# Performance work log

Hardware: AMD Instinct MI355X
Metric: run time of the kernel (lower is better)

## Reference

```python
import jax, jax.numpy as jnp
import numpy as np

# Static config (matches init_kwargs / spatial layout)
SHAPES = ((64, 64), (32, 32), (16, 16))   # (H, W) per level, bev=256 at /4,/8,/16
B, HEADS, LEVELS, POINTS, C = 2, 8, 3, 4, 256
HD = C // HEADS
NV = sum(h * w for h, w in SHAPES)        # 5376
NQ = NV
TP = HEADS * LEVELS * POINTS              # 96


def setup_inputs() -> dict:
    key = jax.random.key(0)
    ks = jax.random.split(key, 10)
    s = 1.0 / np.sqrt(C)
    inp = {
        'query': jax.random.normal(ks[0], (B, NQ, C), dtype=jnp.float32),
        'reference_points': jax.random.uniform(ks[1], (B, NQ, 2), dtype=jnp.float32),
        'value': jax.random.normal(ks[2], (B, NV, C), dtype=jnp.float32),
        'Wv': jax.random.normal(ks[3], (C, C), dtype=jnp.float32) * s,
        'bv': jnp.zeros((C,), dtype=jnp.float32),
        # offset proj: small scale so sampling stays local-ish (orig init is 0)
        'Woff': jax.random.normal(ks[4], (TP * 2, C), dtype=jnp.float32) * (0.02 * s),
        'boff': jnp.zeros((TP * 2,), dtype=jnp.float32),
        'Wa': jax.random.normal(ks[5], (TP, C), dtype=jnp.float32) * s,
        'ba': jnp.zeros((TP,), dtype=jnp.float32),
        'Wo': jax.random.normal(ks[6], (C, C), dtype=jnp.float32) * s,
        'bo': jnp.zeros((C,), dtype=jnp.float32),
    }
    return inp


def _msda(query, reference_points, value, Wv, bv, Woff, boff, Wa, ba, Wo, bo):
    Bb, nq, _ = query.shape
    # value projection -> per-head values
    v = (value @ Wv.T + bv).reshape(Bb, NV, HEADS, HD)
    # sampling offsets: (B, NQ, HEADS, LEVELS, POINTS, 2)
    off = (query @ Woff.T + boff).reshape(Bb, nq, HEADS, LEVELS, POINTS, 2)
    # attention weights: softmax over LEVELS*POINTS jointly
    a = (query @ Wa.T + ba).reshape(Bb, nq, HEADS, LEVELS * POINTS)
    a = jax.nn.softmax(a, axis=-1).reshape(Bb, nq, HEADS, LEVELS, POINTS)
    # sampling locations in [0,1] (clamp matches torch .clamp(0,1))
    loc = jnp.clip(reference_points[:, :, None, None, None, :] + off, 0.0, 1.0)

    out = jnp.zeros((Bb, HEADS, nq, HD), dtype=query.dtype)
    start = 0
    for lvl, (H, W) in enumerate(SHAPES):
        n = H * W
        # (B, HEADS, H*W, HD) flattened level feature map per head
        vl = jnp.transpose(v[:, start:start + n].reshape(Bb, H, W, HEADS, HD),
                           (0, 3, 1, 2, 4)).reshape(Bb, HEADS, n, HD)
        loc_l = loc[:, :, :, lvl]                     # (B, NQ, HEADS, K, 2)
        # align_corners=False unnormalization: ((g+1)*size - 1)/2 with g=2*loc-1
        x = loc_l[..., 0] * W - 0.5
        y = loc_l[..., 1] * H - 0.5
        x0 = jnp.floor(x)
        y0 = jnp.floor(y)
        wx1 = x - x0
        wy1 = y - y0
        x0i = x0.astype(jnp.int32)
        y0i = y0.astype(jnp.int32)
        acc = jnp.zeros((Bb, HEADS, nq * POINTS, HD), dtype=query.dtype)
        for dy in (0, 1):
            for dx in (0, 1):
                ix = x0i + dx
                iy = y0i + dy
                wgt = (wx1 if dx else 1.0 - wx1) * (wy1 if dy else 1.0 - wy1)
                # zero padding outside the map (padding_mode='zeros')
                valid = (ix >= 0) & (ix < W) & (iy >= 0) & (iy < H)
                idx = jnp.clip(iy, 0, H - 1) * W + jnp.clip(ix, 0, W - 1)
                idx_t = jnp.transpose(idx, (0, 2, 1, 3)).reshape(Bb, HEADS, nq * POINTS)
                g = jnp.take_along_axis(vl, idx_t[..., None], axis=2)  # (B,H,NQ*K,HD)
                w_t = jnp.transpose(wgt * valid.astype(wgt.dtype),
                                    (0, 2, 1, 3)).reshape(Bb, HEADS, nq * POINTS, 1)
                acc = acc + g * w_t
        aw = jnp.transpose(a[:, :, :, lvl], (0, 2, 1, 3)).reshape(Bb, HEADS, nq * POINTS, 1)
        out = out + (acc * aw).reshape(Bb, HEADS, nq, POINTS, HD).sum(axis=3)
        start += n
    out = jnp.transpose(out, (0, 2, 1, 3)).reshape(Bb, nq, C)
    return out @ Wo.T + bo


def reference(query, reference_points, value, Wv, bv, Woff, boff, Wa, ba, Wo, bo):
    return _msda(query, reference_points, value, Wv, bv, Woff, boff, Wa, ba, Wo, bo)
```

## Files before the change

### kernel.cpp

```cpp
#include <hip/hip_runtime.h>
#include <hip/hip_bf16.h>
#include <cmath>

#define BATCH   2
#define NQ      5376
#define NV      5376
#define CDIM    256
#define HEADS   8
#define HD      32
#define LEVELS  3
#define POINTS  4
#define TP      96
#define MROWS   (BATCH*NQ)
#define NOFF    (TP*2)
#define NQA     (NOFF+TP)
#define N4_VQ   (MROWS*CDIM/4)

typedef __attribute__((ext_vector_type(8))) short bf16x8;
typedef __attribute__((ext_vector_type(4))) float f32x4;
typedef unsigned short u16;
typedef unsigned int   u32;

#define AS1 __attribute__((address_space(1)))
#define AS3 __attribute__((address_space(3)))

__device__ __forceinline__ void g2lds16(const void* g, void* l) {
    __builtin_amdgcn_global_load_lds((const AS1 void*)g, (AS3 void*)l, 16, 0, 0);
}

__device__ __forceinline__ u16 bf_of(float f) {
    union { __hip_bfloat16 h; u16 s; } u;
    u.h = __float2bfloat16(f);
    return u.s;
}
__device__ __forceinline__ float bf_back(u16 s) {
    return __uint_as_float((u32)s << 16);
}

__global__ __launch_bounds__(256) void split_all_kernel(
    const float* __restrict__ value, const float* __restrict__ query,
    const float* __restrict__ Wv, const float* __restrict__ Woff,
    const float* __restrict__ Wa, const float* __restrict__ Wo,
    u16* __restrict__ vhi, u16* __restrict__ vlo, u16* __restrict__ qhi,
    u16* __restrict__ wv_hi, u16* __restrict__ wv_lo,
    u16* __restrict__ wqa_hi,
    u16* __restrict__ wo_hi, u16* __restrict__ wo_lo)
{
    const int i = blockIdx.x * 256 + threadIdx.x;
    int j; const float* src; u16 *dh, *dl;
    if (i < N4_VQ) {
        j = i; src = value + (size_t)j * 4; dh = vhi; dl = vlo;
    } else if (i < 2 * N4_VQ) {
        j = i - N4_VQ; src = query + (size_t)j * 4; dh = qhi; dl = nullptr;
    } else if (i < 2 * N4_VQ + 16384) {
        j = i - 2 * N4_VQ; src = Wv + (size_t)j * 4; dh = wv_hi; dl = wv_lo;
    } else if (i < 2 * N4_VQ + 34816) {
        j = i - 2 * N4_VQ - 16384;
        const int row = j >> 6, c4 = j & 63;
        src = (row < NOFF) ? (Woff + (size_t)row * CDIM + c4 * 4)
                           : (Wa + (size_t)(row - NOFF) * CDIM + c4 * 4);
        dh = wqa_hi; dl = nullptr;
    } else {
        j = i - 2 * N4_VQ - 34816; src = Wo + (size_t)j * 4; dh = wo_hi; dl = wo_lo;
    }
    const float4 v = *reinterpret_cast<const float4*>(src);
    ushort4 h;
    h.x = bf_of(v.x); h.y = bf_of(v.y); h.z = bf_of(v.z); h.w = bf_of(v.w);
    reinterpret_cast<ushort4*>(dh)[j] = h;
    if (dl) {
        ushort4 l;
        l.x = bf_of(v.x - bf_back(h.x));
        l.y = bf_of(v.y - bf_back(h.y));
        l.z = bf_of(v.z - bf_back(h.z));
        l.w = bf_of(v.w - bf_back(h.w));
        reinterpret_cast<ushort4*>(dl)[j] = l;
    }
}

#define GBM 64
#define GBN 64
#define GBK 32

template <int NPROD, int MODE>
__device__ __forceinline__ void gemm_body(
    int m0, int n0,
    const u16* __restrict__ Ah, const u16* __restrict__ Al,
    const u16* __restrict__ Bh, const u16* __restrict__ Bl,
    const float* __restrict__ bias, const float* __restrict__ bias2,
    void* __restrict__ Cout, void* __restrict__ Cout2,
    int N, int K,
    u16* sAh, u16* sAl, u16* sBh, u16* sBl)
{
    const int tid  = threadIdx.x;
    const int lane = tid & 63;
    const int wave = tid >> 6;
    const int wr   = wave & 1;
    const int wc   = wave >> 1;
    const int qm   = lane & 15;
    const int quad = lane >> 4;

    f32x4 acc[2][2];
    #pragma unroll
    for (int i = 0; i < 2; ++i)
        #pragma unroll
        for (int j = 0; j < 2; ++j)
            acc[i][j] = (f32x4){0.f, 0.f, 0.f, 0.f};

    const int srow = (wave << 4) + (lane >> 2);
    const int sk   = (lane & 3) * 8;
    const int brc  = min(n0 + srow, N - 1);

    for (int k0 = 0; k0 < K; k0 += GBK) {
        const size_t ga = (size_t)(m0 + srow) * K + k0 + sk;
        const size_t gb = (size_t)brc * K + k0 + sk;
        g2lds16(Ah + ga, sAh + wave * 512);
        if (NPROD >= 2) g2lds16(Al + ga, sAl + wave * 512);
        g2lds16(Bh + gb, sBh + wave * 512);
        __syncthreads();

        bf16x8 fah[2], fal[2], fbh[2];
        #pragma unroll
        for (int x = 0; x < 2; ++x) {
            const int rm = wr * 32 + x * 16 + qm;
            const int rn = wc * 32 + x * 16 + qm;
            fah[x] = *reinterpret_cast<const bf16x8*>(&sAh[rm * GBK + quad * 8]);
            fbh[x] = *reinterpret_cast<const bf16x8*>(&sBh[rn * GBK + quad * 8]);
            if (NPROD >= 2)
                fal[x] = *reinterpret_cast<const bf16x8*>(&sAl[rm * GBK + quad * 8]);
        }
        #pragma unroll
        for (int mi = 0; mi < 2; ++mi)
            #pragma unroll
            for (int ni = 0; ni < 2; ++ni) {
                acc[mi][ni] = __builtin_amdgcn_mfma_f32_16x16x32_bf16(
                    fah[mi], fbh[ni], acc[mi][ni], 0, 0, 0);
                if (NPROD >= 2)
                    acc[mi][ni] = __builtin_amdgcn_mfma_f32_16x16x32_bf16(
                        fal[mi], fbh[ni], acc[mi][ni], 0, 0, 0);
            }
        __syncthreads();
    }

    #pragma unroll
    for (int mi = 0; mi < 2; ++mi) {
        #pragma unroll
        for (int ni = 0; ni < 2; ++ni) {
            const int n = n0 + wc * 32 + ni * 16 + qm;
            if (n >= N) continue;
            float bn;
            if (MODE == 2) bn = (n < NOFF) ? bias[n] : bias2[n - NOFF];
            else           bn = bias[n];
            #pragma unroll
            for (int r = 0; r < 4; ++r) {
                const int m = m0 + wr * 32 + mi * 16 + quad * 4 + r;
                const float val = acc[mi][ni][r] + bn;
                if (MODE == 0) {
                    reinterpret_cast<float*>(Cout)[(size_t)m * N + n] = val;
                } else if (MODE == 1) {
                    const int b = m / NV, rr = m - b * NV;
                    const int h = n >> 5, c = n & 31;
                    reinterpret_cast<u16*>(Cout)[
                        (((size_t)b * HEADS + h) * NV + rr) * HD + c] = bf_of(val);
                } else {
                    if (n < NOFF)
                        reinterpret_cast<float*>(Cout)[(size_t)m * NOFF + n] = val;
                    else
                        reinterpret_cast<float*>(Cout2)[(size_t)m * TP + (n - NOFF)] = val;
                }
            }
        }
    }
}

#define VBLOCKS (168 * 4)
__global__ __launch_bounds__(256) void gemm_vqa_kernel(
    const u16* __restrict__ vAh, const u16* __restrict__ vAl,
    const u16* __restrict__ vBh, const float* __restrict__ vbias,
    u16* __restrict__ vOut,
    const u16* __restrict__ qAh, const u16* __restrict__ qBh,
    const float* __restrict__ qb1, const float* __restrict__ qb2,
    float* __restrict__ qOut1, float* __restrict__ qOut2)
{
    __shared__ u16 sAh[GBM * GBK];
    __shared__ u16 sAl[GBM * GBK];
    __shared__ u16 sBh[GBN * GBK];
    const int bid = blockIdx.x;
    if (bid < VBLOCKS) {
        const int nt = bid & 3, mt = bid >> 2;
        gemm_body<2, 1>(mt * GBM, nt * GBN, vAh, vAl, vBh, nullptr,
                        vbias, nullptr, vOut, nullptr, CDIM, CDIM,
                        sAh, sAl, sBh, nullptr);
    } else {
        const int b2 = bid - VBLOCKS;
        const int nt = b2 % 5, mt = b2 / 5;
        gemm_body<1, 2>(mt * GBM, nt * GBN, qAh, nullptr, qBh, nullptr,
                        qb1, qb2, qOut1, qOut2, NQA, CDIM,
                        sAh, sAl, sBh, nullptr);
    }
}

__global__ __launch_bounds__(256) void gemm_out_kernel(
    const u16* __restrict__ Ah, const u16* __restrict__ Al,
    const u16* __restrict__ Bh, const float* __restrict__ bias,
    float* __restrict__ Cout)
{
    __shared__ u16 sAh[GBM * GBK];
    __shared__ u16 sAl[GBM * GBK];
    __shared__ u16 sBh[GBN * GBK];
    const int bid = blockIdx.x;
    const int nt = bid & 3, mt = bid >> 2;
    gemm_body<2, 0>(mt * GBM, nt * GBN, Ah, Al, Bh, nullptr,
                    bias, nullptr, Cout, nullptr, CDIM, CDIM,
                    sAh, sAl, sBh, nullptr);
}

__global__ __launch_bounds__(256) void msda_core_kernel(
    const float* __restrict__ off,
    const float* __restrict__ alog,
    const float* __restrict__ refp,
    const u16*   __restrict__ v,
    u16* __restrict__ t_hi,
    u16* __restrict__ t_lo)
{
    const int tid  = threadIdx.x;
    const int half = tid >> 7;
    const int ht   = tid & 127;
    const int bq   = blockIdx.x * 2 + half;
    const int b    = bq / NQ;

    __shared__ float s_w[2][TP];
    __shared__ int   s_idx[2][TP][4];
    __shared__ float s_twt[2][TP][4];

    if (ht < TP) s_w[half][ht] = alog[(size_t)bq * TP + ht];
    __syncthreads();

    if (ht < HEADS) {
        float mx = -1e30f;
        #pragma unroll
        for (int i = 0; i < 12; ++i) mx = fmaxf(mx, s_w[half][ht * 12 + i]);
        float e[12];
        float sum = 0.f;
        #pragma unroll
        for (int i = 0; i < 12; ++i) {
            e[i] = expf(s_w[half][ht * 12 + i] - mx);
            sum += e[i];
        }
        const float inv = 1.f / sum;
        #pragma unroll
        for (int i = 0; i < 12; ++i) s_w[half][ht * 12 + i] = e[i] * inv;
    }
    __syncthreads();

    if (ht < TP) {
        const int j  = ht;
        const int jj = j % 12;
        const int l  = jj >> 2;
        const int Wl    = (l == 0) ? 64 : (l == 1) ? 32 : 16;
        const int start = (l == 0) ? 0 : (l == 1) ? 4096 : 5120;

        const float refx = refp[(size_t)bq * 2 + 0];
        const float refy = refp[(size_t)bq * 2 + 1];
        const float lx = fminf(fmaxf(refx + off[(size_t)bq * NOFF + j * 2 + 0], 0.f), 1.f) * (float)Wl - 0.5f;
        const float ly = fminf(fmaxf(refy + off[(size_t)bq * NOFF + j * 2 + 1], 0.f), 1.f) * (float)Wl - 0.5f;
        const float fx0 = floorf(lx), fy0 = floorf(ly);
        const int   x0  = (int)fx0,   y0  = (int)fy0;
        const float wx1 = lx - fx0,   wy1 = ly - fy0;
        const float wx0 = 1.f - wx1,  wy0 = 1.f - wy1;
        const float aw  = s_w[half][j];

        #pragma unroll
        for (int k = 0; k < 4; ++k) {
            const int dx = k & 1, dy = k >> 1;
            const int xi = x0 + dx, yi = y0 + dy;
            const bool ok = (xi >= 0) & (xi < Wl) & (yi >= 0) & (yi < Wl);
            const int xc = min(max(xi, 0), Wl - 1);
            const int yc = min(max(yi, 0), Wl - 1);
            s_idx[half][j][k] = (start + yc * Wl + xc) * (HD * 2);
            const float wxy = (dx ? wx1 : wx0) * (dy ? wy1 : wy0);
            s_twt[half][j][k] = ok ? aw * wxy : 0.f;
        }
    }
    __syncthreads();

    const int h   = ht >> 4;
    const int sub = ht & 15;
    const int q   = sub & 7;
    const int rep = sub >> 3;
    const char* vb = (const char*)v + (((size_t)b * HEADS + h) * NV) * (HD * 2) + q * 8;

    float acc0 = 0.f, acc1 = 0.f, acc2 = 0.f, acc3 = 0.f;
    #pragma unroll
    for (int g = 0; g < 3; ++g) {
        uint2 raw[8];
        float wt[8];
        #pragma unroll
        for (int pp = 0; pp < 2; ++pp) {
            const int j = h * 12 + rep * 6 + g * 2 + pp;
            const int4   ix = *reinterpret_cast<const int4*>(&s_idx[half][j][0]);
            const float4 tw = *reinterpret_cast<const float4*>(&s_twt[half][j][0]);
            raw[pp * 4 + 0] = *reinterpret_cast<const uint2*>(vb + ix.x);
            raw[pp * 4 + 1] = *reinterpret_cast<const uint2*>(vb + ix.y);
            raw[pp * 4 + 2] = *reinterpret_cast<const uint2*>(vb + ix.z);
            raw[pp * 4 + 3] = *reinterpret_cast<const uint2*>(vb + ix.w);
            wt[pp * 4 + 0] = tw.x; wt[pp * 4 + 1] = tw.y;
            wt[pp * 4 + 2] = tw.z; wt[pp * 4 + 3] = tw.w;
        }
        #pragma unroll
        for (int k = 0; k < 8; ++k) {
            acc0 += wt[k] * __uint_as_float(raw[k].x << 16);
            acc1 += wt[k] * __uint_as_float(raw[k].x & 0xffff0000u);
            acc2 += wt[k] * __uint_as_float(raw[k].y << 16);
            acc3 += wt[k] * __uint_as_float(raw[k].y & 0xffff0000u);
        }
    }

    acc0 += __shfl_xor(acc0, 8);
    acc1 += __shfl_xor(acc1, 8);
    acc2 += __shfl_xor(acc2, 8);
    acc3 += __shfl_xor(acc3, 8);

    if (rep == 0) {
        ushort4 hh, ll;
        hh.x = bf_of(acc0); ll.x = bf_of(acc0 - bf_back(hh.x));
        hh.y = bf_of(acc1); ll.y = bf_of(acc1 - bf_back(hh.y));
        hh.z = bf_of(acc2); ll.z = bf_of(acc2 - bf_back(hh.z));
        hh.w = bf_of(acc3); ll.w = bf_of(acc3 - bf_back(hh.w));
        const size_t base = (size_t)bq * CDIM + h * HD + q * 4;
        *reinterpret_cast<ushort4*>(t_hi + base) = hh;
        *reinterpret_cast<ushort4*>(t_lo + base) = ll;
    }
}

extern "C" void kernel_launch(void* const* d_in, const int* in_sizes, int n_in,
                              void* d_out, int out_size, void* d_ws, size_t ws_size,
                              hipStream_t stream)
{
    const float* query = (const float*)d_in[0];
    const float* refp  = (const float*)d_in[1];
    const float* value = (const float*)d_in[2];
    const float* Wv    = (const float*)d_in[3];
    const float* bv    = (const float*)d_in[4];
    const float* Woff  = (const float*)d_in[5];
    const float* boff  = (const float*)d_in[6];
    const float* Wa    = (const float*)d_in[7];
    const float* ba    = (const float*)d_in[8];
    const float* Wo    = (const float*)d_in[9];
    const float* bo    = (const float*)d_in[10];
    float* out = (float*)d_out;

    char* w = (char*)d_ws;
    const size_t SZ_QV = (size_t)MROWS * CDIM * 2;
    u16* q_hi   = (u16*)(w);
    u16* val_hi = (u16*)(w + 1 * SZ_QV);
    u16* val_lo = (u16*)(w + 2 * SZ_QV);
    u16* v_bf16 = (u16*)(w + 3 * SZ_QV);
    char* wp    = w + 4 * SZ_QV;
    u16* wv_hi  = (u16*)(wp);                  wp += (size_t)CDIM * CDIM * 2;
    u16* wv_lo  = (u16*)(wp);                  wp += (size_t)CDIM * CDIM * 2;
    u16* wqa_hi = (u16*)(wp);                  wp += (size_t)NQA * CDIM * 2;
    u16* wo_hi  = (u16*)(wp);                  wp += (size_t)CDIM * CDIM * 2;
    u16* wo_lo  = (u16*)(wp);                  wp += (size_t)CDIM * CDIM * 2;
    float* ws_off = (float*)(wp);              wp += (size_t)MROWS * NOFF * 4;
    float* ws_a   = (float*)(wp);
    u16* t_hi = val_hi;
    u16* t_lo = val_lo;

    const dim3 blk(256);

    split_all_kernel<<<dim3((2 * N4_VQ + 51200) / 256), blk, 0, stream>>>(
        value, query, Wv, Woff, Wa, Wo,
        val_hi, val_lo, q_hi, wv_hi, wv_lo, wqa_hi, wo_hi, wo_lo);

    gemm_vqa_kernel<<<dim3(VBLOCKS + (MROWS / GBM) * 5), blk, 0, stream>>>(
        val_hi, val_lo, wv_hi, bv, v_bf16,
        q_hi, wqa_hi, boff, ba, ws_off, ws_a);

    msda_core_kernel<<<dim3(MROWS / 2), blk, 0, stream>>>(
        ws_off, ws_a, refp, v_bf16, t_hi, t_lo);

    gemm_out_kernel<<<dim3((MROWS / GBM) * 4), blk, 0, stream>>>(
        t_hi, t_lo, wo_hi, bo, out);
}
```

Baseline: 140.6 us.

## Fuse fp32-to-bf16 split conversion into GEMM tile loads, store offsets/logits as bf16

Removes the separate split_all kernel. The value/query GEMM and the output GEMM now read fp32 inputs and weights directly and convert them to bf16 hi/lo while staging tiles into LDS. This drops one launch and the round trip of writing and re-reading the bf16 copies. The offset and attention-logit outputs are also stored as bf16 instead of fp32, halving that intermediate traffic at the cost of lower precision in the sampling locations and softmax inputs. In exchange, the async global_load_lds path is replaced by register loads plus conversion for the fused operands, and weights are re-converted in every block.

```diff
diff --git a/kernel.cpp b/kernel.cpp
--- a/kernel.cpp
+++ b/kernel.cpp
@@ -14,7 +14,6 @@
 #define MROWS   (BATCH*NQ)
 #define NOFF    (TP*2)
 #define NQA     (NOFF+TP)
-#define N4_VQ   (MROWS*CDIM/4)
 
 typedef __attribute__((ext_vector_type(8))) short bf16x8;
 typedef __attribute__((ext_vector_type(4))) float f32x4;
@@ -37,60 +36,45 @@
     return __uint_as_float((u32)s << 16);
 }
 
-__global__ __launch_bounds__(256) void split_all_kernel(
-    const float* __restrict__ value, const float* __restrict__ query,
-    const float* __restrict__ Wv, const float* __restrict__ Woff,
-    const float* __restrict__ Wa, const float* __restrict__ Wo,
-    u16* __restrict__ vhi, u16* __restrict__ vlo, u16* __restrict__ qhi,
-    u16* __restrict__ wv_hi, u16* __restrict__ wv_lo,
-    u16* __restrict__ wqa_hi,
-    u16* __restrict__ wo_hi, u16* __restrict__ wo_lo)
-{
-    const int i = blockIdx.x * 256 + threadIdx.x;
-    int j; const float* src; u16 *dh, *dl;
-    if (i < N4_VQ) {
-        j = i; src = value + (size_t)j * 4; dh = vhi; dl = vlo;
-    } else if (i < 2 * N4_VQ) {
-        j = i - N4_VQ; src = query + (size_t)j * 4; dh = qhi; dl = nullptr;
-    } else if (i < 2 * N4_VQ + 16384) {
-        j = i - 2 * N4_VQ; src = Wv + (size_t)j * 4; dh = wv_hi; dl = wv_lo;
-    } else if (i < 2 * N4_VQ + 34816) {
-        j = i - 2 * N4_VQ - 16384;
-        const int row = j >> 6, c4 = j & 63;
-        src = (row < NOFF) ? (Woff + (size_t)row * CDIM + c4 * 4)
-                           : (Wa + (size_t)(row - NOFF) * CDIM + c4 * 4);
-        dh = wqa_hi; dl = nullptr;
-    } else {
-        j = i - 2 * N4_VQ - 34816; src = Wo + (size_t)j * 4; dh = wo_hi; dl = wo_lo;
-    }
-    const float4 v = *reinterpret_cast<const float4*>(src);
+__device__ __forceinline__ ushort4 cvt_hi(float4 v) {
     ushort4 h;
     h.x = bf_of(v.x); h.y = bf_of(v.y); h.z = bf_of(v.z); h.w = bf_of(v.w);
-    reinterpret_cast<ushort4*>(dh)[j] = h;
-    if (dl) {
-        ushort4 l;
-        l.x = bf_of(v.x - bf_back(h.x));
-        l.y = bf_of(v.y - bf_back(h.y));
-        l.z = bf_of(v.z - bf_back(h.z));
-        l.w = bf_of(v.w - bf_back(h.w));
-        reinterpret_cast<ushort4*>(dl)[j] = l;
-    }
+    return h;
+}
+__device__ __forceinline__ ushort4 cvt_lo(float4 v, ushort4 h) {
+    ushort4 l;
+    l.x = bf_of(v.x - bf_back(h.x));
+    l.y = bf_of(v.y - bf_back(h.y));
+    l.z = bf_of(v.z - bf_back(h.z));
+    l.w = bf_of(v.w - bf_back(h.w));
+    return l;
 }
 
 #define GBM 64
 #define GBN 64
 #define GBK 32
 
-template <int NPROD, int MODE>
-__device__ __forceinline__ void gemm_body(
-    int m0, int n0,
-    const u16* __restrict__ Ah, const u16* __restrict__ Al,
-    const u16* __restrict__ Bh, const u16* __restrict__ Bl,
-    const float* __restrict__ bias, const float* __restrict__ bias2,
-    void* __restrict__ Cout, void* __restrict__ Cout2,
-    int N, int K,
-    u16* sAh, u16* sAl, u16* sBh, u16* sBl)
+
+#define VBLOCKS (168 * 4)
+__global__ __launch_bounds__(256) void gemm_vqa_kernel(
+    const float* __restrict__ value, const float* __restrict__ Wv,
+    const float* __restrict__ bv, u16* __restrict__ vOut,
+    const float* __restrict__ query, const float* __restrict__ Woff,
+    const float* __restrict__ Wa,
+    const float* __restrict__ boff, const float* __restrict__ ba,
+    u16* __restrict__ offOut, u16* __restrict__ aOut)
 {
+    __shared__ u16 sAh[GBM * GBK];
+    __shared__ u16 sAl[GBM * GBK];
+    __shared__ u16 sBh[GBN * GBK];
+
+    const int bid = blockIdx.x;
+    const bool vpath = bid < VBLOCKS;
+    int m0, n0;
+    if (vpath) { m0 = (bid >> 2) * GBM;           n0 = (bid & 3) * GBN; }
+    else       { const int b2 = bid - VBLOCKS;
+                 m0 = (b2 / 5) * GBM;             n0 = (b2 % 5) * GBN; }
+
     const int tid  = threadIdx.x;
     const int lane = tid & 63;
     const int wave = tid >> 6;
@@ -99,6 +83,19 @@
     const int qm   = lane & 15;
     const int quad = lane >> 4;
 
+    const int srow = tid >> 2;
+    const int sc   = (tid & 3) * 8;
+
+    const float* Asrc = (vpath ? value : query) + (size_t)(m0 + srow) * CDIM;
+    const float* Bsrc;
+    if (vpath) {
+        Bsrc = Wv + (size_t)(n0 + srow) * CDIM;
+    } else {
+        const int rg = min(n0 + srow, NQA - 1);
+        Bsrc = (rg < NOFF) ? (Woff + (size_t)rg * CDIM)
+                           : (Wa + (size_t)(rg - NOFF) * CDIM);
+    }
+
     f32x4 acc[2][2];
     #pragma unroll
     for (int i = 0; i < 2; ++i)
@@ -106,16 +103,20 @@
         for (int j = 0; j < 2; ++j)
             acc[i][j] = (f32x4){0.f, 0.f, 0.f, 0.f};
 
-    const int srow = (wave << 4) + (lane >> 2);
-    const int sk   = (lane & 3) * 8;
-    const int brc  = min(n0 + srow, N - 1);
-
-    for (int k0 = 0; k0 < K; k0 += GBK) {
-        const size_t ga = (size_t)(m0 + srow) * K + k0 + sk;
-        const size_t gb = (size_t)brc * K + k0 + sk;
-        g2lds16(Ah + ga, sAh + wave * 512);
-        if (NPROD >= 2) g2lds16(Al + ga, sAl + wave * 512);
-        g2lds16(Bh + gb, sBh + wave * 512);
+    for (int k0 = 0; k0 < CDIM; k0 += GBK) {
+        const float4 a0 = *reinterpret_cast<const float4*>(&Asrc[k0 + sc]);
+        const float4 a1 = *reinterpret_cast<const float4*>(&Asrc[k0 + sc + 4]);
+        const ushort4 ah0 = cvt_hi(a0), ah1 = cvt_hi(a1);
+        *reinterpret_cast<ushort4*>(&sAh[srow * GBK + sc])     = ah0;
+        *reinterpret_cast<ushort4*>(&sAh[srow * GBK + sc + 4]) = ah1;
+        if (vpath) {
+            *reinterpret_cast<ushort4*>(&sAl[srow * GBK + sc])     = cvt_lo(a0, ah0);
+            *reinterpret_cast<ushort4*>(&sAl[srow * GBK + sc + 4]) = cvt_lo(a1, ah1);
+        }
+        const float4 b0 = *reinterpret_cast<const float4*>(&Bsrc[k0 + sc]);
+        const float4 b1 = *reinterpret_cast<const float4*>(&Bsrc[k0 + sc + 4]);
+        *reinterpret_cast<ushort4*>(&sBh[srow * GBK + sc])     = cvt_hi(b0);
+        *reinterpret_cast<ushort4*>(&sBh[srow * GBK + sc + 4]) = cvt_hi(b1);
         __syncthreads();
 
         bf16x8 fah[2], fal[2], fbh[2];
@@ -125,7 +126,7 @@
             const int rn = wc * 32 + x * 16 + qm;
             fah[x] = *reinterpret_cast<const bf16x8*>(&sAh[rm * GBK + quad * 8]);
             fbh[x] = *reinterpret_cast<const bf16x8*>(&sBh[rn * GBK + quad * 8]);
-            if (NPROD >= 2)
+            if (vpath)
                 fal[x] = *reinterpret_cast<const bf16x8*>(&sAl[rm * GBK + quad * 8]);
         }
         #pragma unroll
@@ -134,7 +135,7 @@
             for (int ni = 0; ni < 2; ++ni) {
                 acc[mi][ni] = __builtin_amdgcn_mfma_f32_16x16x32_bf16(
                     fah[mi], fbh[ni], acc[mi][ni], 0, 0, 0);
-                if (NPROD >= 2)
+                if (vpath)
                     acc[mi][ni] = __builtin_amdgcn_mfma_f32_16x16x32_bf16(
                         fal[mi], fbh[ni], acc[mi][ni], 0, 0, 0);
             }
@@ -146,77 +147,116 @@
         #pragma unroll
         for (int ni = 0; ni < 2; ++ni) {
             const int n = n0 + wc * 32 + ni * 16 + qm;
-            if (n >= N) continue;
-            float bn;
-            if (MODE == 2) bn = (n < NOFF) ? bias[n] : bias2[n - NOFF];
-            else           bn = bias[n];
-            #pragma unroll
-            for (int r = 0; r < 4; ++r) {
-                const int m = m0 + wr * 32 + mi * 16 + quad * 4 + r;
-                const float val = acc[mi][ni][r] + bn;
-                if (MODE == 0) {
-                    reinterpret_cast<float*>(Cout)[(size_t)m * N + n] = val;
-                } else if (MODE == 1) {
+            if (vpath) {
+                const float bn = bv[n];
+                #pragma unroll
+                for (int r = 0; r < 4; ++r) {
+                    const int m = m0 + wr * 32 + mi * 16 + quad * 4 + r;
+                    const float val = acc[mi][ni][r] + bn;
                     const int b = m / NV, rr = m - b * NV;
                     const int h = n >> 5, c = n & 31;
-                    reinterpret_cast<u16*>(Cout)[
-                        (((size_t)b * HEADS + h) * NV + rr) * HD + c] = bf_of(val);
-                } else {
+                    vOut[(((size_t)b * HEADS + h) * NV + rr) * HD + c] = bf_of(val);
+                }
+            } else {
+                if (n >= NQA) continue;
+                const float bn = (n < NOFF) ? boff[n] : ba[n - NOFF];
+                #pragma unroll
+                for (int r = 0; r < 4; ++r) {
+                    const int m = m0 + wr * 32 + mi * 16 + quad * 4 + r;
+                    const float val = acc[mi][ni][r] + bn;
                     if (n < NOFF)
-                        reinterpret_cast<float*>(Cout)[(size_t)m * NOFF + n] = val;
+                        offOut[(size_t)m * NOFF + n] = bf_of(val);
                     else
-                        reinterpret_cast<float*>(Cout2)[(size_t)m * TP + (n - NOFF)] = val;
+                        aOut[(size_t)m * TP + (n - NOFF)] = bf_of(val);
                 }
             }
         }
     }
 }
 
-#define VBLOCKS (168 * 4)
-__global__ __launch_bounds__(256) void gemm_vqa_kernel(
-    const u16* __restrict__ vAh, const u16* __restrict__ vAl,
-    const u16* __restrict__ vBh, const float* __restrict__ vbias,
-    u16* __restrict__ vOut,
-    const u16* __restrict__ qAh, const u16* __restrict__ qBh,
-    const float* __restrict__ qb1, const float* __restrict__ qb2,
-    float* __restrict__ qOut1, float* __restrict__ qOut2)
-{
-    __shared__ u16 sAh[GBM * GBK];
-    __shared__ u16 sAl[GBM * GBK];
-    __shared__ u16 sBh[GBN * GBK];
-    const int bid = blockIdx.x;
-    if (bid < VBLOCKS) {
-        const int nt = bid & 3, mt = bid >> 2;
-        gemm_body<2, 1>(mt * GBM, nt * GBN, vAh, vAl, vBh, nullptr,
-                        vbias, nullptr, vOut, nullptr, CDIM, CDIM,
-                        sAh, sAl, sBh, nullptr);
-    } else {
-        const int b2 = bid - VBLOCKS;
-        const int nt = b2 % 5, mt = b2 / 5;
-        gemm_body<1, 2>(mt * GBM, nt * GBN, qAh, nullptr, qBh, nullptr,
-                        qb1, qb2, qOut1, qOut2, NQA, CDIM,
-                        sAh, sAl, sBh, nullptr);
-    }
-}
-
 __global__ __launch_bounds__(256) void gemm_out_kernel(
     const u16* __restrict__ Ah, const u16* __restrict__ Al,
-    const u16* __restrict__ Bh, const float* __restrict__ bias,
+    const float* __restrict__ Wo, const float* __restrict__ bias,
     float* __restrict__ Cout)
 {
     __shared__ u16 sAh[GBM * GBK];
     __shared__ u16 sAl[GBM * GBK];
     __shared__ u16 sBh[GBN * GBK];
+
     const int bid = blockIdx.x;
-    const int nt = bid & 3, mt = bid >> 2;
-    gemm_body<2, 0>(mt * GBM, nt * GBN, Ah, Al, Bh, nullptr,
-                    bias, nullptr, Cout, nullptr, CDIM, CDIM,
-                    sAh, sAl, sBh, nullptr);
+    const int m0 = (bid >> 2) * GBM;
+    const int n0 = (bid & 3) * GBN;
+
+    const int tid  = threadIdx.x;
+    const int lane = tid & 63;
+    const int wave = tid >> 6;
+    const int wr   = wave & 1;
+    const int wc   = wave >> 1;
+    const int qm   = lane & 15;
+    const int quad = lane >> 4;
+
+    const int arow = (wave << 4) + (lane >> 2);
+    const int ak   = (lane & 3) * 8;
+    const int srow = tid >> 2;
+    const int sc   = (tid & 3) * 8;
+    const float* Bsrc = Wo + (size_t)(n0 + srow) * CDIM;
+
+    f32x4 acc[2][2];
+    #pragma unroll
+    for (int i = 0; i < 2; ++i)
+        #pragma unroll
+        for (int j = 0; j < 2; ++j)
+            acc[i][j] = (f32x4){0.f, 0.f, 0.f, 0.f};
+
+    for (int k0 = 0; k0 < CDIM; k0 += GBK) {
+        const size_t ga = (size_t)(m0 + arow) * CDIM + k0 + ak;
+        g2lds16(Ah + ga, sAh + wave * 512);
+        g2lds16(Al + ga, sAl + wave * 512);
+        const float4 b0 = *reinterpret_cast<const float4*>(&Bsrc[k0 + sc]);
+        const float4 b1 = *reinterpret_cast<const float4*>(&Bsrc[k0 + sc + 4]);
+        *reinterpret_cast<ushort4*>(&sBh[srow * GBK + sc])     = cvt_hi(b0);
+        *reinterpret_cast<ushort4*>(&sBh[srow * GBK + sc + 4]) = cvt_hi(b1);
+        __syncthreads();
+
+        bf16x8 fah[2], fal[2], fbh[2];
+        #pragma unroll
+        for (int x = 0; x < 2; ++x) {
+            const int rm = wr * 32 + x * 16 + qm;
+            const int rn = wc * 32 + x * 16 + qm;
+            fah[x] = *reinterpret_cast<const bf16x8*>(&sAh[rm * GBK + quad * 8]);
+            fal[x] = *reinterpret_cast<const bf16x8*>(&sAl[rm * GBK + quad * 8]);
+            fbh[x] = *reinterpret_cast<const bf16x8*>(&sBh[rn * GBK + quad * 8]);
+        }
+        #pragma unroll
+        for (int mi = 0; mi < 2; ++mi)
+            #pragma unroll
+            for (int ni = 0; ni < 2; ++ni) {
+                acc[mi][ni] = __builtin_amdgcn_mfma_f32_16x16x32_bf16(
+                    fah[mi], fbh[ni], acc[mi][ni], 0, 0, 0);
+                acc[mi][ni] = __builtin_amdgcn_mfma_f32_16x16x32_bf16(
+                    fal[mi], fbh[ni], acc[mi][ni], 0, 0, 0);
+            }
+        __syncthreads();
+    }
+
+    #pragma unroll
+    for (int mi = 0; mi < 2; ++mi) {
+        #pragma unroll
+        for (int ni = 0; ni < 2; ++ni) {
+            const int n = n0 + wc * 32 + ni * 16 + qm;
+            const float bn = bias[n];
+            #pragma unroll
+            for (int r = 0; r < 4; ++r) {
+                const int m = m0 + wr * 32 + mi * 16 + quad * 4 + r;
+                Cout[(size_t)m * CDIM + n] = acc[mi][ni][r] + bn;
+            }
+        }
+    }
 }
 
 __global__ __launch_bounds__(256) void msda_core_kernel(
-    const float* __restrict__ off,
-    const float* __restrict__ alog,
+    const u16* __restrict__ off,
+    const u16* __restrict__ alog,
     const float* __restrict__ refp,
     const u16*   __restrict__ v,
     u16* __restrict__ t_hi,
@@ -232,7 +272,7 @@
     __shared__ int   s_idx[2][TP][4];
     __shared__ float s_twt[2][TP][4];
 
-    if (ht < TP) s_w[half][ht] = alog[(size_t)bq * TP + ht];
+    if (ht < TP) s_w[half][ht] = bf_back(alog[(size_t)bq * TP + ht]);
     __syncthreads();
 
     if (ht < HEADS) {
@@ -261,8 +301,10 @@
 
         const float refx = refp[(size_t)bq * 2 + 0];
         const float refy = refp[(size_t)bq * 2 + 1];
-        const float lx = fminf(fmaxf(refx + off[(size_t)bq * NOFF + j * 2 + 0], 0.f), 1.f) * (float)Wl - 0.5f;
-        const float ly = fminf(fmaxf(refy + off[(size_t)bq * NOFF + j * 2 + 1], 0.f), 1.f) * (float)Wl - 0.5f;
+        const float ox = bf_back(off[(size_t)bq * NOFF + j * 2 + 0]);
+        const float oy = bf_back(off[(size_t)bq * NOFF + j * 2 + 1]);
+        const float lx = fminf(fmaxf(refx + ox, 0.f), 1.f) * (float)Wl - 0.5f;
+        const float ly = fminf(fmaxf(refy + oy, 0.f), 1.f) * (float)Wl - 0.5f;
         const float fx0 = floorf(lx), fy0 = floorf(ly);
         const int   x0  = (int)fx0,   y0  = (int)fy0;
         const float wx1 = lx - fx0,   wy1 = ly - fy0;
@@ -350,35 +392,22 @@
     float* out = (float*)d_out;
 
     char* w = (char*)d_ws;
-    const size_t SZ_QV = (size_t)MROWS * CDIM * 2;
-    u16* q_hi   = (u16*)(w);
-    u16* val_hi = (u16*)(w + 1 * SZ_QV);
-    u16* val_lo = (u16*)(w + 2 * SZ_QV);
-    u16* v_bf16 = (u16*)(w + 3 * SZ_QV);
-    char* wp    = w + 4 * SZ_QV;
-    u16* wv_hi  = (u16*)(wp);                  wp += (size_t)CDIM * CDIM * 2;
-    u16* wv_lo  = (u16*)(wp);                  wp += (size_t)CDIM * CDIM * 2;
-    u16* wqa_hi = (u16*)(wp);                  wp += (size_t)NQA * CDIM * 2;
-    u16* wo_hi  = (u16*)(wp);                  wp += (size_t)CDIM * CDIM * 2;
-    u16* wo_lo  = (u16*)(wp);                  wp += (size_t)CDIM * CDIM * 2;
-    float* ws_off = (float*)(wp);              wp += (size_t)MROWS * NOFF * 4;
-    float* ws_a   = (float*)(wp);
-    u16* t_hi = val_hi;
-    u16* t_lo = val_lo;
+    const size_t SZ_T = (size_t)MROWS * CDIM * 2;
+    u16* v_bf16 = (u16*)(w);
+    u16* t_hi   = (u16*)(w + 1 * SZ_T);
+    u16* t_lo   = (u16*)(w + 2 * SZ_T);
+    u16* ws_off = (u16*)(w + 3 * SZ_T);
+    u16* ws_a   = (u16*)(w + 3 * SZ_T + (size_t)MROWS * NOFF * 2);
 
     const dim3 blk(256);
 
-    split_all_kernel<<<dim3((2 * N4_VQ + 51200) / 256), blk, 0, stream>>>(
-        value, query, Wv, Woff, Wa, Wo,
-        val_hi, val_lo, q_hi, wv_hi, wv_lo, wqa_hi, wo_hi, wo_lo);
-
     gemm_vqa_kernel<<<dim3(VBLOCKS + (MROWS / GBM) * 5), blk, 0, stream>>>(
-        val_hi, val_lo, wv_hi, bv, v_bf16,
-        q_hi, wqa_hi, boff, ba, ws_off, ws_a);
+        value, Wv, bv, v_bf16,
+        query, Woff, Wa, boff, ba, ws_off, ws_a);
 
     msda_core_kernel<<<dim3(MROWS / 2), blk, 0, stream>>>(
         ws_off, ws_a, refp, v_bf16, t_hi, t_lo);
 
     gemm_out_kernel<<<dim3((MROWS / GBM) * 4), blk, 0, stream>>>(
-        t_hi, t_lo, wo_hi, bo, out);
-}
+        t_hi, t_lo, Wo, bo, out);
+}
```

Measured after the change: 138.9 us. No clear change (-1.2%).
